# Optimization experiments

Measured on AMD Instinct MI355X. Metric: run time of the kernel, lower is better.

## Reference

```python
import jax, jax.numpy as jnp
import numpy as np

EMB = 128
NUM_RADIAL = 6
NUM_DENSE = 3
NUM_TARGETS = 12
N_EDGES = 640000
N_ATOMS = 20000


def setup_inputs() -> dict:
    key = jax.random.key(0)
    ks = jax.random.split(key, 12)
    inp = {
        "x": jax.random.normal(ks[0], (N_EDGES, EMB), dtype=jnp.float32),
        "rbf": jax.random.normal(ks[1], (N_EDGES, NUM_RADIAL), dtype=jnp.float32),
        "idnb_i": jax.random.randint(ks[2], (N_EDGES,), 0, N_ATOMS, dtype=jnp.int64),
        "n_atoms": N_ATOMS,
        # parameters
        "W_rbf": jax.random.normal(ks[3], (NUM_RADIAL, EMB), dtype=jnp.float32) * 0.1,  # no bias
        "dense_Ws": jax.random.normal(ks[4], (NUM_DENSE, EMB, EMB), dtype=jnp.float32) * (1.0 / np.sqrt(EMB)),
        "dense_bs": jax.random.normal(ks[5], (NUM_DENSE, EMB), dtype=jnp.float32) * 0.01,
        "W_final": jax.random.normal(ks[6], (EMB, NUM_TARGETS), dtype=jnp.float32) * (1.0 / np.sqrt(EMB)),  # no bias
    }
    return inp


def reference(x, rbf, idnb_i, n_atoms, W_rbf, dense_Ws, dense_bs, W_final):
    # gate: dense_rbf(rbf) * x, fused elementwise
    g = rbf @ W_rbf                      # [E, emb]
    xg = g * x                           # [E, emb]
    # scatter_add over edge -> atom indices
    h = jax.ops.segment_sum(xg, idnb_i, num_segments=n_atoms)  # [n_atoms, emb]
    # dense MLP head with swish activation
    for i in range(NUM_DENSE):
        h = jax.nn.silu(h @ dense_Ws[i] + dense_bs[i])
    return h @ W_final                   # [n_atoms, num_targets]
```

## Files before the change

### kernel.cpp

```cpp
#include <hip/hip_runtime.h>

#define EMB 128
#define NRAD 6
#define NT 12
#define NE 640000
#define NA 20000
#define SLOTS 128
#define HS_LD (EMB + 4)

__global__ __launch_bounds__(256) void zero_cnt(int* __restrict__ cnt) {
    int i = blockIdx.x * 256 + threadIdx.x;
    if (i < NA) cnt[i] = 0;
}

__global__ __launch_bounds__(256) void scatter_perm(const int* __restrict__ idx,
                                                    int* __restrict__ cnt,
                                                    int* __restrict__ perm) {
    int e = blockIdx.x * 256 + threadIdx.x;
    if (e < NE) {
        int a = idx[e];
        int pos = atomicAdd(&cnt[a], 1);
        if (pos < SLOTS) perm[(long long)a * SLOTS + pos] = e;
    }
}

__global__ __launch_bounds__(64) void gather_h(
    const float* __restrict__ x, const float* __restrict__ rbf,
    const float* __restrict__ Wrbf, const int* __restrict__ perm,
    const int* __restrict__ cnt, float* __restrict__ h)
{
    int a = blockIdx.x, t = threadIdx.x;
    float2 w[NRAD];
    #pragma unroll
    for (int i = 0; i < NRAD; ++i)
        w[i] = *reinterpret_cast<const float2*>(&Wrbf[i * EMB + 2 * t]);

    int n = cnt[a]; if (n > SLOTS) n = SLOTS;
    const int* prow = perm + (long long)a * SLOTS;

    float2 acc[4];
    #pragma unroll
    for (int i = 0; i < 4; ++i) acc[i] = make_float2(0.f, 0.f);

    auto body = [&](int j, float2& ac) {
        int edge = prow[j];
        const float* rp = rbf + (long long)edge * NRAD;
        float2 r01 = *reinterpret_cast<const float2*>(rp);
        float2 r23 = *reinterpret_cast<const float2*>(rp + 2);
        float2 r45 = *reinterpret_cast<const float2*>(rp + 4);
        float g0, g1;
        g0 = r01.x * w[0].x;            g1 = r01.x * w[0].y;
        g0 = fmaf(r01.y, w[1].x, g0);   g1 = fmaf(r01.y, w[1].y, g1);
        g0 = fmaf(r23.x, w[2].x, g0);   g1 = fmaf(r23.x, w[2].y, g1);
        g0 = fmaf(r23.y, w[3].x, g0);   g1 = fmaf(r23.y, w[3].y, g1);
        g0 = fmaf(r45.x, w[4].x, g0);   g1 = fmaf(r45.x, w[4].y, g1);
        g0 = fmaf(r45.y, w[5].x, g0);   g1 = fmaf(r45.y, w[5].y, g1);
        float2 xv = *reinterpret_cast<const float2*>(&x[(long long)edge * EMB + 2 * t]);
        ac.x = fmaf(g0, xv.x, ac.x);
        ac.y = fmaf(g1, xv.y, ac.y);
    };

    int j = 0;
    for (; j + 3 < n; j += 4) {
        body(j, acc[0]); body(j + 1, acc[1]); body(j + 2, acc[2]); body(j + 3, acc[3]);
    }
    for (; j < n; ++j) body(j, acc[0]);

    float2 r = {acc[0].x + acc[1].x + acc[2].x + acc[3].x,
                acc[0].y + acc[1].y + acc[2].y + acc[3].y};
    *reinterpret_cast<float2*>(&h[(long long)a * EMB + 2 * t]) = r;
}

__global__ __launch_bounds__(256) void mlp_head(
    const float* __restrict__ h, const float* __restrict__ Ws,
    const float* __restrict__ bs, const float* __restrict__ Wf,
    float* __restrict__ out)
{
    __shared__ float hs[32][HS_LD];
    __shared__ float wt[16 * EMB];

    const int t  = threadIdx.x;
    const int ab = blockIdx.x * 32;

    for (int i = t; i < 32 * 32; i += 256) {
        int row = i >> 5, c4 = (i & 31) << 2;
        *reinterpret_cast<float4*>(&hs[row][c4]) =
            *reinterpret_cast<const float4*>(&h[(long long)(ab + row) * EMB + c4]);
    }

    const int jg = t & 31, j0 = jg * 4;
    const int ag = t >> 5, a0 = ag * 4;
    __syncthreads();

    for (int l = 0; l < 3; ++l) {
        float acc[4][4];
        #pragma unroll
        for (int ai = 0; ai < 4; ++ai)
            #pragma unroll
            for (int ji = 0; ji < 4; ++ji) acc[ai][ji] = bs[l * EMB + j0 + ji];

        const float* W = Ws + (long long)l * EMB * EMB;
        for (int kt = 0; kt < 8; ++kt) {
            __syncthreads();
            {
                const float4* wsrc = reinterpret_cast<const float4*>(W + kt * 16 * EMB);
                float4* wdst = reinterpret_cast<float4*>(wt);
                wdst[t]       = wsrc[t];
                wdst[t + 256] = wsrc[t + 256];
            }
            __syncthreads();
            #pragma unroll
            for (int kk = 0; kk < 16; ++kk) {
                float4 wv = *reinterpret_cast<const float4*>(&wt[kk * EMB + j0]);
                #pragma unroll
                for (int ai = 0; ai < 4; ++ai) {
                    float hv = hs[a0 + ai][kt * 16 + kk];
                    acc[ai][0] = fmaf(hv, wv.x, acc[ai][0]);
                    acc[ai][1] = fmaf(hv, wv.y, acc[ai][1]);
                    acc[ai][2] = fmaf(hv, wv.z, acc[ai][2]);
                    acc[ai][3] = fmaf(hv, wv.w, acc[ai][3]);
                }
            }
        }
        __syncthreads();
        #pragma unroll
        for (int ai = 0; ai < 4; ++ai) {
            #pragma unroll
            for (int ji = 0; ji < 4; ++ji) {
                float z = acc[ai][ji];
                acc[ai][ji] = z / (1.f + __expf(-z));
            }
            float4 v = make_float4(acc[ai][0], acc[ai][1], acc[ai][2], acc[ai][3]);
            *reinterpret_cast<float4*>(&hs[a0 + ai][j0]) = v;
        }
        __syncthreads();
    }

    for (int i = t; i < EMB * NT / 4; i += 256)
        reinterpret_cast<float4*>(wt)[i] = reinterpret_cast<const float4*>(Wf)[i];
    __syncthreads();

    for (int i = t; i < 32 * NT; i += 256) {
        int a = i / NT, jj = i - a * NT;
        float s = 0.f;
        #pragma unroll 4
        for (int k = 0; k < EMB; ++k) s = fmaf(hs[a][k], wt[k * NT + jj], s);
        out[(long long)(ab + a) * NT + jj] = s;
    }
}

extern "C" void kernel_launch(void* const* d_in, const int* in_sizes, int n_in,
                              void* d_out, int out_size, void* d_ws, size_t ws_size,
                              hipStream_t stream) {
    const float* x    = (const float*)d_in[0];
    const float* rbf  = (const float*)d_in[1];
    const int*   idx  = (const int*)d_in[2];
    const float* Wrbf = (const float*)d_in[4];
    const float* Ws   = (const float*)d_in[5];
    const float* bsp  = (const float*)d_in[6];
    const float* Wf   = (const float*)d_in[7];
    float* out = (float*)d_out;

    char* ws = (char*)d_ws;
    float* h    = (float*)ws;
    int*   cnt  = (int*)(ws + (size_t)NA * EMB * 4);
    int*   perm = cnt + 20032;

    zero_cnt    <<<(NA + 255) / 256, 256, 0, stream>>>(cnt);
    scatter_perm<<<(NE + 255) / 256, 256, 0, stream>>>(idx, cnt, perm);
    gather_h    <<<NA, 64, 0, stream>>>(x, rbf, Wrbf, perm, cnt, h);
    mlp_head    <<<NA / 32, 256, 0, stream>>>(h, Ws, bsp, Wf, out);
}
```

Measured before the change: 162.6 us.

## Double-buffer MLP weight tiles, pack four atoms per gather block, memset counters

The MLP head now double-buffers the 16-row weight tiles in shared memory, prefetching the next tile across layer boundaries so there is one barrier per tile instead of two. Its inner loop is unrolled by four, using float4 reads of the hidden state and vectorised bias loads. The gather kernel packs four atoms per 256-thread block instead of one per 64-thread block, and the counter-zeroing kernel is replaced by hipMemsetAsync. The goal is less launch and barrier overhead and better latency hiding, at the cost of extra shared memory and more register pressure.

```diff
diff --git a/kernel.cpp b/kernel.cpp
--- a/kernel.cpp
+++ b/kernel.cpp
@@ -7,11 +7,6 @@
 #define NA 20000
 #define SLOTS 128
 #define HS_LD (EMB + 4)
-
-__global__ __launch_bounds__(256) void zero_cnt(int* __restrict__ cnt) {
-    int i = blockIdx.x * 256 + threadIdx.x;
-    if (i < NA) cnt[i] = 0;
-}
 
 __global__ __launch_bounds__(256) void scatter_perm(const int* __restrict__ idx,
                                                     int* __restrict__ cnt,
@@ -24,12 +19,15 @@
     }
 }
 
-__global__ __launch_bounds__(64) void gather_h(
+__global__ __launch_bounds__(256) void gather_h(
     const float* __restrict__ x, const float* __restrict__ rbf,
     const float* __restrict__ Wrbf, const int* __restrict__ perm,
     const int* __restrict__ cnt, float* __restrict__ h)
 {
-    int a = blockIdx.x, t = threadIdx.x;
+    int wid = threadIdx.x >> 6;
+    int a   = blockIdx.x * 4 + wid;
+    int t   = threadIdx.x & 63;
+
     float2 w[NRAD];
     #pragma unroll
     for (int i = 0; i < NRAD; ++i)
@@ -77,7 +75,7 @@
     float* __restrict__ out)
 {
     __shared__ float hs[32][HS_LD];
-    __shared__ float wt[16 * EMB];
+    __shared__ float wt[2][16 * EMB];
 
     const int t  = threadIdx.x;
     const int ab = blockIdx.x * 32;
@@ -88,37 +86,55 @@
             *reinterpret_cast<const float4*>(&h[(long long)(ab + row) * EMB + c4]);
     }
 
+    auto load_tile = [&](int g, int buf) {
+        const float4* s4 = reinterpret_cast<const float4*>(Ws + (long long)g * 16 * EMB);
+        float4* wdst = reinterpret_cast<float4*>(wt[buf]);
+        wdst[t]       = s4[t];
+        wdst[t + 256] = s4[t + 256];
+    };
+    load_tile(0, 0);
+
     const int jg = t & 31, j0 = jg * 4;
     const int ag = t >> 5, a0 = ag * 4;
-    __syncthreads();
 
     for (int l = 0; l < 3; ++l) {
+        float4 bv = *reinterpret_cast<const float4*>(&bs[l * EMB + j0]);
         float acc[4][4];
         #pragma unroll
-        for (int ai = 0; ai < 4; ++ai)
+        for (int ai = 0; ai < 4; ++ai) {
+            acc[ai][0] = bv.x; acc[ai][1] = bv.y; acc[ai][2] = bv.z; acc[ai][3] = bv.w;
+        }
+
+        for (int kt = 0; kt < 8; ++kt) {
+            int g = l * 8 + kt;
+            __syncthreads();
+            if (g + 1 < 24) load_tile(g + 1, (g + 1) & 1);
+            const float* wtc = wt[g & 1];
             #pragma unroll
-            for (int ji = 0; ji < 4; ++ji) acc[ai][ji] = bs[l * EMB + j0 + ji];
-
-        const float* W = Ws + (long long)l * EMB * EMB;
-        for (int kt = 0; kt < 8; ++kt) {
-            __syncthreads();
-            {
-                const float4* wsrc = reinterpret_cast<const float4*>(W + kt * 16 * EMB);
-                float4* wdst = reinterpret_cast<float4*>(wt);
-                wdst[t]       = wsrc[t];
-                wdst[t + 256] = wsrc[t + 256];
-            }
-            __syncthreads();
-            #pragma unroll
-            for (int kk = 0; kk < 16; ++kk) {
-                float4 wv = *reinterpret_cast<const float4*>(&wt[kk * EMB + j0]);
+            for (int q = 0; q < 4; ++q) {
+                float4 w0 = *reinterpret_cast<const float4*>(&wtc[(q * 4 + 0) * EMB + j0]);
+                float4 w1 = *reinterpret_cast<const float4*>(&wtc[(q * 4 + 1) * EMB + j0]);
+                float4 w2 = *reinterpret_cast<const float4*>(&wtc[(q * 4 + 2) * EMB + j0]);
+                float4 w3 = *reinterpret_cast<const float4*>(&wtc[(q * 4 + 3) * EMB + j0]);
                 #pragma unroll
                 for (int ai = 0; ai < 4; ++ai) {
-                    float hv = hs[a0 + ai][kt * 16 + kk];
-                    acc[ai][0] = fmaf(hv, wv.x, acc[ai][0]);
-                    acc[ai][1] = fmaf(hv, wv.y, acc[ai][1]);
-                    acc[ai][2] = fmaf(hv, wv.z, acc[ai][2]);
-                    acc[ai][3] = fmaf(hv, wv.w, acc[ai][3]);
+                    float4 hv = *reinterpret_cast<const float4*>(&hs[a0 + ai][kt * 16 + q * 4]);
+                    acc[ai][0] = fmaf(hv.x, w0.x, acc[ai][0]);
+                    acc[ai][1] = fmaf(hv.x, w0.y, acc[ai][1]);
+                    acc[ai][2] = fmaf(hv.x, w0.z, acc[ai][2]);
+                    acc[ai][3] = fmaf(hv.x, w0.w, acc[ai][3]);
+                    acc[ai][0] = fmaf(hv.y, w1.x, acc[ai][0]);
+                    acc[ai][1] = fmaf(hv.y, w1.y, acc[ai][1]);
+                    acc[ai][2] = fmaf(hv.y, w1.z, acc[ai][2]);
+                    acc[ai][3] = fmaf(hv.y, w1.w, acc[ai][3]);
+                    acc[ai][0] = fmaf(hv.z, w2.x, acc[ai][0]);
+                    acc[ai][1] = fmaf(hv.z, w2.y, acc[ai][1]);
+                    acc[ai][2] = fmaf(hv.z, w2.z, acc[ai][2]);
+                    acc[ai][3] = fmaf(hv.z, w2.w, acc[ai][3]);
+                    acc[ai][0] = fmaf(hv.w, w3.x, acc[ai][0]);
+                    acc[ai][1] = fmaf(hv.w, w3.y, acc[ai][1]);
+                    acc[ai][2] = fmaf(hv.w, w3.z, acc[ai][2]);
+                    acc[ai][3] = fmaf(hv.w, w3.w, acc[ai][3]);
                 }
             }
         }
@@ -133,18 +149,18 @@
             float4 v = make_float4(acc[ai][0], acc[ai][1], acc[ai][2], acc[ai][3]);
             *reinterpret_cast<float4*>(&hs[a0 + ai][j0]) = v;
         }
-        __syncthreads();
     }
 
+    __syncthreads();
     for (int i = t; i < EMB * NT / 4; i += 256)
-        reinterpret_cast<float4*>(wt)[i] = reinterpret_cast<const float4*>(Wf)[i];
+        reinterpret_cast<float4*>(wt[0])[i] = reinterpret_cast<const float4*>(Wf)[i];
     __syncthreads();
 
     for (int i = t; i < 32 * NT; i += 256) {
         int a = i / NT, jj = i - a * NT;
         float s = 0.f;
         #pragma unroll 4
-        for (int k = 0; k < EMB; ++k) s = fmaf(hs[a][k], wt[k * NT + jj], s);
+        for (int k = 0; k < EMB; ++k) s = fmaf(hs[a][k], wt[0][k * NT + jj], s);
         out[(long long)(ab + a) * NT + jj] = s;
     }
 }
@@ -166,8 +182,8 @@
     int*   cnt  = (int*)(ws + (size_t)NA * EMB * 4);
     int*   perm = cnt + 20032;
 
-    zero_cnt    <<<(NA + 255) / 256, 256, 0, stream>>>(cnt);
+    hipMemsetAsync(cnt, 0, (size_t)NA * sizeof(int), stream);
     scatter_perm<<<(NE + 255) / 256, 256, 0, stream>>>(idx, cnt, perm);
-    gather_h    <<<NA, 64, 0, stream>>>(x, rbf, Wrbf, perm, cnt, h);
+    gather_h    <<<NA / 4, 256, 0, stream>>>(x, rbf, Wrbf, perm, cnt, h);
     mlp_head    <<<NA / 32, 256, 0, stream>>>(h, Ws, bsp, Wf, out);
 }
```

Result: slower. 201.2 us (+23.8%).
